# Performance work log

Measured on AMD Instinct MI355X. Metric: run time of the kernel, lower is better.

The kernel has to match this reference:

```python
import jax, jax.numpy as jnp
import numpy as np

B, L, C = 2, 2048, 2048
H, HKV, D = 16, 4, 128  # heads, kv heads, head_dim
G = H // HKV            # GQA group size
NEG = -1e9


def rms_norm(x, w, eps=1e-6):
    # FastRMSNorm: compute in fp32, scale by weight, cast back
    xf = x.astype(jnp.float32)
    y = xf * jax.lax.rsqrt(jnp.mean(xf * xf, axis=-1, keepdims=True) + eps) * w
    return y.astype(x.dtype)


def apply_rope(t, cos, sin):
    # t: (B, h, L, D); cos/sin: (L, D//2) broadcast to (1,1,L,D//2)
    t1, t2 = jnp.split(t, 2, axis=-1)
    c = cos[None, None]
    s = sin[None, None]
    return jnp.concatenate([t1 * c - t2 * s, t2 * c + t1 * s], axis=-1)


def setup_inputs() -> dict:
    key = jax.random.key(0)
    ks = jax.random.split(key, 8)
    x = jax.random.normal(ks[0], (B, L, C), jnp.float32)
    Wq = jax.random.normal(ks[1], (H * D, C), jnp.float32) * 0.02
    Wk = jax.random.normal(ks[2], (HKV * D, C), jnp.float32) * 0.02
    Wv = jax.random.normal(ks[3], (HKV * D, C), jnp.float32) * 0.02
    Wo = jax.random.normal(ks[4], (C, H * D), jnp.float32) * 0.02
    q_norm_w = jnp.ones((D,), jnp.float32)
    k_norm_w = jnp.ones((D,), jnp.float32)
    pos = jnp.arange(L, dtype=jnp.float32)[:, None]
    inv_freq = 1.0 / (10000.0 ** (jnp.arange(0, D, 2, dtype=jnp.float32) / D))
    ang = pos * inv_freq[None, :]            # (L, D//2)
    rope_cos = jnp.cos(ang)
    rope_sin = jnp.sin(ang)
    # VAR-style block-causal visibility: 8 blocks of 256, query block i sees key blocks <= i
    blk = jnp.arange(L) // 256
    vis = blk[None, :] <= blk[:, None]       # (L, L) bool
    attn_bias = jnp.where(vis, 0.0, NEG).astype(jnp.float32)[None, None]  # (1,1,L,L)
    return dict(x=x, Wq=Wq, Wk=Wk, Wv=Wv, Wo=Wo, q_norm_w=q_norm_w,
                k_norm_w=k_norm_w, rope_cos=rope_cos, rope_sin=rope_sin,
                attn_bias=attn_bias)


def reference(x, Wq, Wk, Wv, Wo, q_norm_w, k_norm_w, rope_cos, rope_sin, attn_bias):
    b, l, c = x.shape
    # fused projections -> (B, h, L, D)
    q = rms_norm((x @ Wq.T).reshape(b, l, H, D), q_norm_w).transpose(0, 2, 1, 3)
    k = rms_norm((x @ Wk.T).reshape(b, l, HKV, D), k_norm_w).transpose(0, 2, 1, 3)
    v = (x @ Wv.T).reshape(b, l, HKV, D).transpose(0, 2, 1, 3)
    q = apply_rope(q, rope_cos, rope_sin)
    k = apply_rope(k, rope_cos, rope_sin)
    scale = D ** -0.5
    # GQA: group query heads over kv heads
    qg = q.reshape(b, HKV, G, l, D)
    scores = jnp.einsum('bkgqd,bkKd->bkgqK', qg, k) * scale
    scores = scores + attn_bias[:, :, None]  # broadcast (1,1,1,L,L)
    probs = jax.nn.softmax(scores, axis=-1)
    out = jnp.einsum('bkgqK,bkKd->bkgqd', probs, v)
    out = out.reshape(b, H, l, D).transpose(0, 2, 1, 3).reshape(b, l, H * D)
    return out @ Wo.T
```

## Files before the change

kernel.cpp:

```cpp
#include <hip/hip_runtime.h>

#define B_ 2
#define L_ 2048
#define C_ 2048
#define H_ 16
#define HKV_ 4
#define D_ 128
#define G_ (H_ / HKV_)
#define TOK_ (B_ * L_)
#define NQKV_ 3072

typedef __bf16 bf16;
typedef __bf16 bf16x4 __attribute__((ext_vector_type(4)));
typedef __bf16 bf16x8 __attribute__((ext_vector_type(8)));
typedef float f32x4 __attribute__((ext_vector_type(4)));

__device__ inline void gload16(const void* g, void* l) {
  __builtin_amdgcn_global_load_lds(
      (const __attribute__((address_space(1))) void*)g,
      (__attribute__((address_space(3))) void*)l, 16, 0, 0);
}

#define N4_X  2097152
#define N4_WQ 1048576
#define N4_WK 262144
#define N4_WV 262144
#define N4_WO 1048576
#define N4_TOT (N4_X + N4_WQ + N4_WK + N4_WV + N4_WO)

__global__ void cvt_all(const float* __restrict__ x, const float* __restrict__ wq,
                        const float* __restrict__ wk, const float* __restrict__ wv,
                        const float* __restrict__ wo, bf16* __restrict__ dst) {
  int stride = gridDim.x * blockDim.x;
  for (int j = blockIdx.x * blockDim.x + threadIdx.x; j < N4_TOT; j += stride) {
    const float* s;
    int off;
    if (j < N4_X) { s = x; off = j; }
    else if (j < N4_X + N4_WQ) { s = wq; off = j - N4_X; }
    else if (j < N4_X + N4_WQ + N4_WK) { s = wk; off = j - (N4_X + N4_WQ); }
    else if (j < N4_X + N4_WQ + N4_WK + N4_WV) { s = wv; off = j - (N4_X + N4_WQ + N4_WK); }
    else { s = wo; off = j - (N4_X + N4_WQ + N4_WK + N4_WV); }
    float4 v = reinterpret_cast<const float4*>(s)[off];
    bf16x4 o = {(bf16)v.x, (bf16)v.y, (bf16)v.z, (bf16)v.w};
    reinterpret_cast<bf16x4*>(dst)[j] = o;
  }
}

template <bool OUT_F32>
__global__ __launch_bounds__(256, 3) void gemm_bt(
    const bf16* __restrict__ A, const bf16* __restrict__ Bm,
    void* __restrict__ Cm, int M, int N, int K) {
  __shared__ __align__(16) bf16 sA[3][128 * 32];
  __shared__ __align__(16) bf16 sB[3][128 * 32];
  const int tid = threadIdx.x;
  const int row0 = blockIdx.x * 128, col0 = blockIdx.y * 128;
  const int wid = tid >> 6, lane = tid & 63;
  const int wr = wid >> 1, wc = wid & 1;
  const int l15 = lane & 15, kk = (lane >> 4) * 8;
  f32x4 acc[4][4] = {};
  const int nk = K / 32;
  const int r0 = tid >> 2, c0 = tid & 3;
  const int r1 = 64 + r0, c1 = c0;
  const int ldsA0 = (wid * 64) * 8, ldsA1 = (256 + wid * 64) * 8;

  auto stage = [&](int kt, int slot) {
    gload16(A + (size_t)(row0 + r0) * K + kt * 32 + c0 * 8, &sA[slot][ldsA0]);
    gload16(A + (size_t)(row0 + r1) * K + kt * 32 + c1 * 8, &sA[slot][ldsA1]);
    gload16(Bm + (size_t)(col0 + r0) * K + kt * 32 + c0 * 8, &sB[slot][ldsA0]);
    gload16(Bm + (size_t)(col0 + r1) * K + kt * 32 + c1 * 8, &sB[slot][ldsA1]);
  };

  stage(0, 0);
  stage(1, 1);
  asm volatile("s_waitcnt vmcnt(4)" ::: "memory");
  __builtin_amdgcn_s_barrier();
  __builtin_amdgcn_sched_barrier(0);

  int slot = 0;
  for (int kt = 0; kt < nk; ++kt) {
    int s2 = slot + 2; if (s2 >= 3) s2 -= 3;
    if (kt + 2 < nk) stage(kt + 2, s2);
    const bf16* cA = sA[slot];
    const bf16* cB = sB[slot];
    bf16x8 af[4], bfr[4];
#pragma unroll
    for (int m = 0; m < 4; ++m)
      af[m] = *reinterpret_cast<const bf16x8*>(cA + (wr * 64 + m * 16 + l15) * 32 + kk);
#pragma unroll
    for (int n = 0; n < 4; ++n)
      bfr[n] = *reinterpret_cast<const bf16x8*>(cB + (wc * 64 + n * 16 + l15) * 32 + kk);
    __builtin_amdgcn_s_setprio(1);
#pragma unroll
    for (int m = 0; m < 4; ++m)
#pragma unroll
      for (int n = 0; n < 4; ++n)
        acc[m][n] = __builtin_amdgcn_mfma_f32_16x16x32_bf16(af[m], bfr[n], acc[m][n], 0, 0, 0);
    __builtin_amdgcn_s_setprio(0);
    if (kt + 2 < nk)
      asm volatile("s_waitcnt vmcnt(4)" ::: "memory");
    else
      asm volatile("s_waitcnt vmcnt(0)" ::: "memory");
    __builtin_amdgcn_s_barrier();
    __builtin_amdgcn_sched_barrier(0);
    slot = (slot + 1 == 3) ? 0 : slot + 1;
  }
#pragma unroll
  for (int m = 0; m < 4; ++m)
#pragma unroll
    for (int n = 0; n < 4; ++n)
#pragma unroll
      for (int r = 0; r < 4; ++r) {
        int row = row0 + wr * 64 + m * 16 + (lane >> 4) * 4 + r;
        int col = col0 + wc * 64 + n * 16 + l15;
        if constexpr (OUT_F32)
          reinterpret_cast<float*>(Cm)[(size_t)row * N + col] = acc[m][n][r];
        else
          reinterpret_cast<bf16*>(Cm)[(size_t)row * N + col] = (bf16)acc[m][n][r];
      }
}

__global__ __launch_bounds__(256) void knorm_vtrans(
    const bf16* __restrict__ proj,
    const float* __restrict__ normw,
    const float* __restrict__ cosb, const float* __restrict__ sinb,
    bf16* __restrict__ kout,
    bf16* __restrict__ vt) {
  __shared__ __align__(16) bf16 sT[64 * 136];
  if (blockIdx.x < 4096) {
    int wid = (blockIdx.x * blockDim.x + threadIdx.x) >> 6;
    int lane = threadIdx.x & 63;
    int head = wid & 3, tok = wid >> 2;
    int b = tok / L_, l = tok % L_;
    const bf16* p = proj + (size_t)tok * NQKV_ + H_ * D_ + head * D_;
    float t1 = (float)p[lane];
    float t2 = (float)p[lane + 64];
    float ss = t1 * t1 + t2 * t2;
#pragma unroll
    for (int off = 32; off; off >>= 1) ss += __shfl_xor(ss, off);
    float r = rsqrtf(ss * (1.0f / 128.0f) + 1e-6f);
    float n1 = t1 * r * normw[lane];
    float n2 = t2 * r * normw[lane + 64];
    float c = cosb[l * 64 + lane], s = sinb[l * 64 + lane];
    bf16* q = kout + (((size_t)b * HKV_ + head) * L_ + l) * D_;
    q[lane] = (bf16)(n1 * c - n2 * s);
    q[lane + 64] = (bf16)(n2 * c + n1 * s);
    return;
  }
  const int vbid = blockIdx.x - 4096;
  const int t = threadIdx.x;
  const int l0 = (vbid & 31) * 64;
  const int bk = vbid >> 5;
  const bf16* src = proj + (size_t)((bk >> 2) * L_ + l0) * NQKV_ + (H_ + HKV_) * D_ + (bk & 3) * D_;
#pragma unroll
  for (int c = 0; c < 4; ++c) {
    int idx = c * 256 + t;
    int l = idx >> 4, dc = idx & 15;
    bf16x8 v = *reinterpret_cast<const bf16x8*>(src + (size_t)l * NQKV_ + dc * 8);
    *reinterpret_cast<bf16x8*>((char*)sT + l * 272 + ((dc ^ (l >> 3)) << 4)) = v;
  }
  __syncthreads();
  bf16* dst = vt + (size_t)bk * D_ * L_ + l0;
#pragma unroll
  for (int c = 0; c < 4; ++c) {
    int idx = c * 256 + t;
    int d = idx >> 3, lg = idx & 7;
    bf16x8 o;
#pragma unroll
    for (int j = 0; j < 8; ++j) {
      int l = lg * 8 + j;
      o[j] = *reinterpret_cast<const bf16*>((char*)sT + l * 272 + (((d >> 3) ^ lg) << 4) + (d & 7) * 2);
    }
    *reinterpret_cast<bf16x8*>(dst + (size_t)d * L_ + lg * 8) = o;
  }
}

#define SM_K0 0
#define SM_K1 16384
#define SM_V0 32768
#define SM_V1 49152
#define SM_P  65536
__global__ __launch_bounds__(512, 4) void attn_fused(
    const bf16* __restrict__ QKV,
    const bf16* __restrict__ Kn,
    const bf16* __restrict__ Vt,
    const float* __restrict__ qnw,
    const float* __restrict__ cosb, const float* __restrict__ sinb,
    bf16* __restrict__ AO) {
  __shared__ __align__(16) char smem[81920];
  const int tid = threadIdx.x;
  const int wid = tid >> 6, lane = tid & 63;
  const int bid = blockIdx.x;
  const int bk = bid & 7;
  const int qt = (bid < 256) ? (bid >> 3) : 63 - ((bid - 256) >> 3);
  const int b = bk >> 2;
  const int hl = wid & 3, qs = wid >> 2;
  const int h = (bk & 3) * G_ + hl;
  const int qrow0 = qt * 32 + qs * 16;
  const int l15 = lane & 15, g4 = lane >> 4, kk = g4 * 8;
  const int swz = (l15 & 7) << 4;

  const int qrow = qrow0 + l15;
  const bf16* qsrc = QKV + (size_t)(b * L_ + qrow) * NQKV_ + h * D_;
  float t[4][8];
  float ss = 0.f;
#pragma unroll
  for (int c = 0; c < 4; ++c) {
    bf16x8 v = *reinterpret_cast<const bf16x8*>(qsrc + c * 32 + kk);
#pragma unroll
    for (int j = 0; j < 8; ++j) { t[c][j] = (float)v[j]; ss += t[c][j] * t[c][j]; }
  }

  const int kr0 = tid >> 4, kc0 = tid & 15;
  const int kr1 = 32 + kr0;
  const int vr0 = tid >> 3, vc0 = tid & 7;
  const int vr1 = 64 + vr0;
  const bf16* kb = Kn + (size_t)bk * L_ * D_;
  const bf16* vb = Vt + (size_t)bk * D_ * (size_t)L_;
  const bf16* kp0 = kb + (size_t)kr0 * D_ + ((kc0 ^ (kr0 & 7)) * 8);
  const bf16* kp1 = kb + (size_t)kr1 * D_ + ((kc0 ^ (kr1 & 7)) * 8);
  const bf16* vp0 = vb + (size_t)vr0 * L_ + ((vc0 ^ (vr0 & 7)) * 8);
  const bf16* vp1 = vb + (size_t)vr1 * L_ + ((vc0 ^ (vr1 & 7)) * 8);

  const int ntiles = ((qt >> 3) + 1) * 4;
  gload16(kp0, smem + SM_K0 + tid * 16);
  gload16(kp1, smem + SM_K0 + 8192 + tid * 16);
  gload16(vp0, smem + SM_V0 + tid * 16);
  gload16(vp1, smem + SM_V0 + 8192 + tid * 16);

  constexpr float SCL = 0.12752650038632816f;
  ss += __shfl_xor(ss, 16);
  ss += __shfl_xor(ss, 32);
  const float rr = rsqrtf(ss * (1.0f / 128.0f) + 1e-6f);
  bf16x8 qf[4];
#pragma unroll
  for (int c = 0; c < 2; ++c)
#pragma unroll
    for (int j = 0; j < 8; ++j) {
      int i = c * 32 + kk + j;
      float n1 = t[c][j] * rr * qnw[i];
      float n2 = t[c + 2][j] * rr * qnw[i + 64];
      float cs = cosb[qrow * 64 + i], sn = sinb[qrow * 64 + i];
      qf[c][j] = (bf16)((n1 * cs - n2 * sn) * SCL);
      qf[c + 2][j] = (bf16)((n2 * cs + n1 * sn) * SCL);
    }

  int aK[4], aV[2], aPw[4];
#pragma unroll
  for (int c = 0; c < 4; ++c)
    aK[c] = l15 * 256 + ((((c << 2) + g4) ^ (l15 & 7)) << 4);
#pragma unroll
  for (int hh = 0; hh < 2; ++hh)
    aV[hh] = l15 * 128 + ((((hh << 2) + g4) ^ (l15 & 7)) << 4);
  const int pbase = SM_P + wid * 2048 + l15 * 128;
#pragma unroll
  for (int n = 0; n < 4; ++n)
    aPw[n] = pbase + (((n << 5) + (g4 << 3)) ^ swz);
  const int aPr0 = pbase + ((g4 << 4) ^ swz);
  const int aPr1 = pbase + ((64 + (g4 << 4)) ^ swz);

  f32x4 acc[8] = {};
  float mref = -1e30f, lpart = 0.f;

  __syncthreads();

  auto tile_step = [&](int KB, int VB, int KBn, int VBn, int ktNext, bool doPref) {
    if (doPref) {
      gload16(kp0 + (size_t)ktNext * 64 * D_, smem + KBn + tid * 16);
      gload16(kp1 + (size_t)ktNext * 64 * D_, smem + KBn + 8192 + tid * 16);
      gload16(vp0 + ktNext * 64, smem + VBn + tid * 16);
      gload16(vp1 + ktNext * 64, smem + VBn + 8192 + tid * 16);
    }
    f32x4 s[4];
    __builtin_amdgcn_s_setprio(1);
#pragma unroll
    for (int n = 0; n < 4; ++n) {
      f32x4 st = {};
#pragma unroll
      for (int c = 0; c < 4; ++c) {
        bf16x8 kf = *reinterpret_cast<const bf16x8*>(smem + KB + n * 4096 + aK[c]);
        st = __builtin_amdgcn_mfma_f32_16x16x32_bf16(kf, qf[c], st, 0, 0, 0);
      }
      s[n] = st;
    }
    __builtin_amdgcn_s_setprio(0);
    float pm = fmaxf(fmaxf(s[0][0], s[0][1]), fmaxf(s[0][2], s[0][3]));
#pragma unroll
    for (int n = 1; n < 4; ++n)
      pm = fmaxf(pm, fmaxf(fmaxf(s[n][0], s[n][1]), fmaxf(s[n][2], s[n][3])));
    if (!__all(pm <= mref + 8.f)) {
      pm = fmaxf(pm, __shfl_xor(pm, 16));
      pm = fmaxf(pm, __shfl_xor(pm, 32));
      float mnew = fmaxf(mref, pm);
      float resc = exp2f(mref - mnew);
      mref = mnew;
      lpart *= resc;
#pragma unroll
      for (int f = 0; f < 8; ++f) acc[f] *= resc;
    }
    float qsum[4];
#pragma unroll
    for (int n = 0; n < 4; ++n) {
      float p0 = exp2f(s[n][0] - mref);
      float p1 = exp2f(s[n][1] - mref);
      float p2 = exp2f(s[n][2] - mref);
      float p3 = exp2f(s[n][3] - mref);
      bf16x4 pw = {(bf16)p0, (bf16)p1, (bf16)p2, (bf16)p3};
      *reinterpret_cast<bf16x4*>(smem + aPw[n]) = pw;
      qsum[n] = (p0 + p1) + (p2 + p3);
    }
    lpart += (qsum[0] + qsum[1]) + (qsum[2] + qsum[3]);
    bf16x8 pf0 = *reinterpret_cast<const bf16x8*>(smem + aPr0);
    bf16x8 pf1 = *reinterpret_cast<const bf16x8*>(smem + aPr1);
    __builtin_amdgcn_s_setprio(1);
#pragma unroll
    for (int f = 0; f < 8; ++f) {
      bf16x8 vf0 = *reinterpret_cast<const bf16x8*>(smem + VB + f * 2048 + aV[0]);
      acc[f] = __builtin_amdgcn_mfma_f32_16x16x32_bf16(vf0, pf0, acc[f], 0, 0, 0);
      bf16x8 vf1 = *reinterpret_cast<const bf16x8*>(smem + VB + f * 2048 + aV[1]);
      acc[f] = __builtin_amdgcn_mfma_f32_16x16x32_bf16(vf1, pf1, acc[f], 0, 0, 0);
    }
    __builtin_amdgcn_s_setprio(0);
    __syncthreads();
  };

  for (int kt = 0; kt < ntiles; kt += 2) {
    tile_step(SM_K0, SM_V0, SM_K1, SM_V1, kt + 1, true);
    tile_step(SM_K1, SM_V1, SM_K0, SM_V0, kt + 2, kt + 2 < ntiles);
  }

  lpart += __shfl_xor(lpart, 16);
  lpart += __shfl_xor(lpart, 32);
  const float rinv = 1.f / lpart;
  bf16* aop = AO + ((size_t)(b * L_ + qrow0 + l15) * H_ + h) * D_ + (g4 << 2);
#pragma unroll
  for (int f = 0; f < 8; ++f) {
    bf16x4 o = {(bf16)(acc[f][0] * rinv), (bf16)(acc[f][1] * rinv),
                (bf16)(acc[f][2] * rinv), (bf16)(acc[f][3] * rinv)};
    *reinterpret_cast<bf16x4*>(aop + f * 16) = o;
  }
}

extern "C" void kernel_launch(void* const* d_in, const int* in_sizes, int n_in,
                              void* d_out, int out_size, void* d_ws, size_t ws_size,
                              hipStream_t stream) {
  const float* x = (const float*)d_in[0];
  const float* Wq = (const float*)d_in[1];
  const float* Wk = (const float*)d_in[2];
  const float* Wv = (const float*)d_in[3];
  const float* Wo = (const float*)d_in[4];
  const float* qnw = (const float*)d_in[5];
  const float* knw = (const float*)d_in[6];
  const float* rc = (const float*)d_in[7];
  const float* rs = (const float*)d_in[8];
  float* out = (float*)d_out;

  char* ws = (char*)d_ws;
  bf16* xb = (bf16*)ws;    ws += (size_t)TOK_ * C_ * 2;
  bf16* wqb = (bf16*)ws;   ws += (size_t)(H_ * D_) * C_ * 2;
  bf16* wkb = (bf16*)ws;   ws += (size_t)(HKV_ * D_) * C_ * 2;
  bf16* wvb = (bf16*)ws;   ws += (size_t)(HKV_ * D_) * C_ * 2;
  bf16* wob = (bf16*)ws;   ws += (size_t)C_ * (H_ * D_) * 2;
  bf16* qkv = (bf16*)ws;   ws += (size_t)TOK_ * NQKV_ * 2;
  bf16* Kb = (bf16*)ws;    ws += (size_t)TOK_ * HKV_ * D_ * 2;
  bf16* Vtb = (bf16*)ws;   ws += (size_t)TOK_ * HKV_ * D_ * 2;
  bf16* AOb = xb;

  cvt_all<<<2048, 256, 0, stream>>>(x, Wq, Wk, Wv, Wo, xb);

  gemm_bt<false><<<dim3(TOK_ / 128, NQKV_ / 128), 256, 0, stream>>>(
      xb, wqb, qkv, TOK_, NQKV_, C_);

  knorm_vtrans<<<4352, 256, 0, stream>>>(qkv, knw, rc, rs, Kb, Vtb);

  attn_fused<<<512, 512, 0, stream>>>(qkv, Kb, Vtb, qnw, rc, rs, AOb);

  gemm_bt<true><<<dim3(TOK_ / 128, C_ / 128), 256, 0, stream>>>(
      AOb, wob, out, TOK_, C_, H_ * D_);
}
```

Baseline: 199.2 us.

## Switch GEMM to double-buffered LDS with higher occupancy; vectorize K norm/RoPE

The GEMM drops from a three-stage to a two-stage LDS pipeline and raises the launch-bounds occupancy hint from 3 to 4 blocks per CU. It now waits for all outstanding loads each iteration, so prefetch depth falls from two tiles to one in exchange for more resident waves. Separately, the K RMSNorm+RoPE path loads and stores bf16 pairs per lane and gets the rotation partner through a lane shuffle, replacing scalar strided accesses.

Measured after the change: 197.5 us. No clear change (-0.8%).

```diff
diff --git a/kernel.cpp b/kernel.cpp
--- a/kernel.cpp
+++ b/kernel.cpp
@@ -11,6 +11,7 @@
 #define NQKV_ 3072
 
 typedef __bf16 bf16;
+typedef __bf16 bf16x2 __attribute__((ext_vector_type(2)));
 typedef __bf16 bf16x4 __attribute__((ext_vector_type(4)));
 typedef __bf16 bf16x8 __attribute__((ext_vector_type(8)));
 typedef float f32x4 __attribute__((ext_vector_type(4)));
@@ -47,11 +48,11 @@
 }
 
 template <bool OUT_F32>
-__global__ __launch_bounds__(256, 3) void gemm_bt(
+__global__ __launch_bounds__(256, 4) void gemm_bt(
     const bf16* __restrict__ A, const bf16* __restrict__ Bm,
     void* __restrict__ Cm, int M, int N, int K) {
-  __shared__ __align__(16) bf16 sA[3][128 * 32];
-  __shared__ __align__(16) bf16 sB[3][128 * 32];
+  __shared__ __align__(16) bf16 sA[2][128 * 32];
+  __shared__ __align__(16) bf16 sB[2][128 * 32];
   const int tid = threadIdx.x;
   const int row0 = blockIdx.x * 128, col0 = blockIdx.y * 128;
   const int wid = tid >> 6, lane = tid & 63;
@@ -71,17 +72,15 @@
   };
 
   stage(0, 0);
-  stage(1, 1);
-  asm volatile("s_waitcnt vmcnt(4)" ::: "memory");
+  asm volatile("s_waitcnt vmcnt(0)" ::: "memory");
   __builtin_amdgcn_s_barrier();
   __builtin_amdgcn_sched_barrier(0);
 
-  int slot = 0;
   for (int kt = 0; kt < nk; ++kt) {
-    int s2 = slot + 2; if (s2 >= 3) s2 -= 3;
-    if (kt + 2 < nk) stage(kt + 2, s2);
-    const bf16* cA = sA[slot];
-    const bf16* cB = sB[slot];
+    const int cur = kt & 1;
+    if (kt + 1 < nk) stage(kt + 1, cur ^ 1);
+    const bf16* cA = sA[cur];
+    const bf16* cB = sB[cur];
     bf16x8 af[4], bfr[4];
 #pragma unroll
     for (int m = 0; m < 4; ++m)
@@ -96,13 +95,11 @@
       for (int n = 0; n < 4; ++n)
         acc[m][n] = __builtin_amdgcn_mfma_f32_16x16x32_bf16(af[m], bfr[n], acc[m][n], 0, 0, 0);
     __builtin_amdgcn_s_setprio(0);
-    if (kt + 2 < nk)
-      asm volatile("s_waitcnt vmcnt(4)" ::: "memory");
-    else
+    if (kt + 1 < nk) {
       asm volatile("s_waitcnt vmcnt(0)" ::: "memory");
-    __builtin_amdgcn_s_barrier();
-    __builtin_amdgcn_sched_barrier(0);
-    slot = (slot + 1 == 3) ? 0 : slot + 1;
+      __builtin_amdgcn_s_barrier();
+      __builtin_amdgcn_sched_barrier(0);
+    }
   }
 #pragma unroll
   for (int m = 0; m < 4; ++m)
@@ -127,23 +124,35 @@
     bf16* __restrict__ vt) {
   __shared__ __align__(16) bf16 sT[64 * 136];
   if (blockIdx.x < 4096) {
-    int wid = (blockIdx.x * blockDim.x + threadIdx.x) >> 6;
+    int gw = (blockIdx.x * blockDim.x + threadIdx.x) >> 6;
     int lane = threadIdx.x & 63;
-    int head = wid & 3, tok = wid >> 2;
+    int head = gw & 3, tok = gw >> 2;
     int b = tok / L_, l = tok % L_;
     const bf16* p = proj + (size_t)tok * NQKV_ + H_ * D_ + head * D_;
-    float t1 = (float)p[lane];
-    float t2 = (float)p[lane + 64];
-    float ss = t1 * t1 + t2 * t2;
+    bf16x2 v = *reinterpret_cast<const bf16x2*>(p + 2 * lane);
+    float t0 = (float)v[0], t1 = (float)v[1];
+    float ss = t0 * t0 + t1 * t1;
 #pragma unroll
     for (int off = 32; off; off >>= 1) ss += __shfl_xor(ss, off);
     float r = rsqrtf(ss * (1.0f / 128.0f) + 1e-6f);
-    float n1 = t1 * r * normw[lane];
-    float n2 = t2 * r * normw[lane + 64];
-    float c = cosb[l * 64 + lane], s = sinb[l * 64 + lane];
+    float2 w = *reinterpret_cast<const float2*>(normw + 2 * lane);
+    float n0 = t0 * r * w.x, n1 = t1 * r * w.y;
+    float pn0 = __shfl_xor(n0, 32);
+    float pn1 = __shfl_xor(n1, 32);
+    int ci = (2 * lane) & 63;
+    float2 c2 = *reinterpret_cast<const float2*>(cosb + l * 64 + ci);
+    float2 s2 = *reinterpret_cast<const float2*>(sinb + l * 64 + ci);
+    float o0, o1;
+    if (lane < 32) {
+      o0 = n0 * c2.x - pn0 * s2.x;
+      o1 = n1 * c2.y - pn1 * s2.y;
+    } else {
+      o0 = n0 * c2.x + pn0 * s2.x;
+      o1 = n1 * c2.y + pn1 * s2.y;
+    }
+    bf16x2 o = {(bf16)o0, (bf16)o1};
     bf16* q = kout + (((size_t)b * HKV_ + head) * L_ + l) * D_;
-    q[lane] = (bf16)(n1 * c - n2 * s);
-    q[lane + 64] = (bf16)(n2 * c + n1 * s);
+    *reinterpret_cast<bf16x2*>(q + 2 * lane) = o;
     return;
   }
   const int vbid = blockIdx.x - 4096;
```
